# Optimization experiments

Measured on AMD Instinct MI355X. Metric: run time of the kernel, lower is better.

The kernel has to match this reference:

```python
import jax, jax.numpy as jnp
import numpy as np

N_NODES = 50000
N_EDGES = 1600000
N_GRAPHS = 512
IN_DIM = 384
HID = 128


def gcn_conv(x, W, b, src, dst, n_nodes):
    # PyG GCNConv: h = W^T x, then propagate with sym norm over A + I (self-loops).
    h = x @ W  # [N, out]
    # self-loops
    loop = jnp.arange(n_nodes, dtype=src.dtype)
    s = jnp.concatenate([src, loop])
    d = jnp.concatenate([dst, loop])
    ones = jnp.ones(s.shape[0], dtype=h.dtype)
    deg = jax.ops.segment_sum(ones, d, num_segments=n_nodes)  # in-degree incl self-loop
    dis = jnp.where(deg > 0, jax.lax.rsqrt(deg), 0.0)
    norm = dis[s] * dis[d]  # [E+N]
    msg = h[s] * norm[:, None]  # gather + scale
    out = jax.ops.segment_sum(msg, d, num_segments=n_nodes)  # scatter-add
    return out + b


def global_mean_pool(x, batch, num_graphs):
    sums = jax.ops.segment_sum(x, batch, num_segments=num_graphs)
    cnt = jax.ops.segment_sum(jnp.ones(x.shape[0], dtype=x.dtype), batch, num_segments=num_graphs)
    return sums / jnp.maximum(cnt, 1.0)[:, None]


def setup_inputs() -> dict:
    key = jax.random.key(0)
    ks = jax.random.split(key, 12)
    x = jax.random.normal(ks[0], (N_NODES, IN_DIM), dtype=jnp.float32)
    edge_index = jax.random.randint(ks[1], (2, N_EDGES), 0, N_NODES, dtype=jnp.int64 if jax.config.jax_enable_x64 else jnp.int32)
    batch = jnp.sort(jax.random.randint(ks[2], (N_NODES,), 0, N_GRAPHS, dtype=jnp.int32))
    def glorot(k, shape):
        lim = float(np.sqrt(6.0 / (shape[0] + shape[1])))
        return jax.random.uniform(k, shape, jnp.float32, -lim, lim)
    return {
        "x": x,
        "edge_index": edge_index,
        "batch": batch,
        "W1": glorot(ks[3], (IN_DIM, HID)),
        "b1": jnp.zeros((HID,), jnp.float32),
        "W2": glorot(ks[4], (HID, HID)),
        "b2": jnp.zeros((HID,), jnp.float32),
        "Wl1": glorot(ks[5], (HID, HID // 2)),
        "bl1": jnp.zeros((HID // 2,), jnp.float32),
        "Wl2": glorot(ks[6], (HID // 2, 5)),
        "bl2": jnp.zeros((5,), jnp.float32),
    }


def reference(x, edge_index, batch, W1, b1, W2, b2, Wl1, bl1, Wl2, bl2):
    src, dst = edge_index[0], edge_index[1]
    n = x.shape[0]
    h = jax.nn.relu(gcn_conv(x, W1, b1, src, dst, n))
    h = jax.nn.relu(gcn_conv(h, W2, b2, src, dst, n))
    g = global_mean_pool(h, batch, N_GRAPHS)  # [G, HID]
    g = jax.nn.relu(g @ Wl1 + bl1)
    return jax.nn.sigmoid(g @ Wl2 + bl2)  # [G, 5]
```

## Files before the change

kernel.cpp:

```cpp
#include <hip/hip_runtime.h>
#include <hip/hip_bf16.h>
#include <string.h>

#define HID 128
#define NGRAPH 512
#define IN_DIM 384

typedef __attribute__((ext_vector_type(2))) float f32x2;

__device__ __forceinline__ float bf2f(unsigned short u) {
    unsigned int x = ((unsigned int)u) << 16;
    float f; __builtin_memcpy(&f, &x, 4); return f;
}
__device__ __forceinline__ unsigned short f2bf(float f) {
    unsigned int b; __builtin_memcpy(&b, &f, 4);
    unsigned int r = (b + 0x7FFFu + ((b >> 16) & 1u)) >> 16;
    return (unsigned short)r;
}

__global__ void deg_kernel(const int* __restrict__ dst, int* __restrict__ deg, int E) {
    int e = blockIdx.x * blockDim.x + threadIdx.x;
    if (e < E) atomicAdd(&deg[dst[e]], 1);
}

__global__ void dis_kernel(const int* __restrict__ deg, float* __restrict__ dis, int n) {
    int v = blockIdx.x * blockDim.x + threadIdx.x;
    if (v < n) dis[v] = rsqrtf((float)(deg[v] + 1));
}

__global__ __launch_bounds__(256) void scan_part(const int* __restrict__ deg, int* __restrict__ row,
                                                 int* __restrict__ blockSums, int n) {
    __shared__ int ts[256];
    const int b = blockIdx.x, t = threadIdx.x;
    const int base = b * 1024 + t * 4;
    int v0 = (base + 0 < n) ? deg[base + 0] : 0;
    int v1 = (base + 1 < n) ? deg[base + 1] : 0;
    int v2 = (base + 2 < n) ? deg[base + 2] : 0;
    int v3 = (base + 3 < n) ? deg[base + 3] : 0;
    const int s = v0 + v1 + v2 + v3;
    ts[t] = s;
    __syncthreads();
    for (int off = 1; off < 256; off <<= 1) {
        int x = (t >= off) ? ts[t - off] : 0;
        __syncthreads();
        ts[t] += x;
        __syncthreads();
    }
    int p = ts[t] - s;
    if (base + 0 < n) { row[base + 0] = p; p += v0; }
    if (base + 1 < n) { row[base + 1] = p; p += v1; }
    if (base + 2 < n) { row[base + 2] = p; p += v2; }
    if (base + 3 < n) { row[base + 3] = p; }
    if (t == 255) blockSums[b] = ts[255];
}

__global__ void scan_tops(int* __restrict__ blockSums, int nb) {
    if (threadIdx.x == 0 && blockIdx.x == 0) {
        int acc = 0;
        for (int i = 0; i < nb; i++) { int v = blockSums[i]; blockSums[i] = acc; acc += v; }
    }
}

__global__ __launch_bounds__(256) void scan_add(int* __restrict__ row, int* __restrict__ cursor,
                                                const int* __restrict__ blockSums, int n, int E) {
    const int b = blockIdx.x, t = threadIdx.x;
    const int off = blockSums[b];
    const int base = b * 1024 + t * 4;
#pragma unroll
    for (int j = 0; j < 4; j++) {
        int i = base + j;
        if (i < n) { int v = row[i] + off; row[i] = v; cursor[i] = v; }
    }
    if (b == 0 && t == 0) row[n] = E;
}

__global__ void fill_kernel(const int* __restrict__ src, const int* __restrict__ dst,
                            int* __restrict__ cursor, unsigned short* __restrict__ csr16,
                            int E, int lo, int hi) {
    int e = blockIdx.x * blockDim.x + threadIdx.x;
    if (e < E) {
        const int d = dst[e];
        if (d >= lo && d < hi) {
            int pos = atomicAdd(&cursor[d], 1);
            csr16[pos] = (unsigned short)src[e];
        }
    }
}

template <int K, bool BF16IN>
__global__ __launch_bounds__(256) void gemm_tile(const void* __restrict__ Xv,
                                                 const float* __restrict__ W,
                                                 const float* __restrict__ dis,
                                                 unsigned int* __restrict__ out8, int n) {
    constexpr int KC = 32;
    __shared__ float asT[KC][68];
    __shared__ float bs[KC * HID];
    const int t = threadIdx.x;
    const int tx = t & 31;
    const int ty = t >> 5;
    const int row0 = blockIdx.x * 64;

    float4 acc[8];
#pragma unroll
    for (int j = 0; j < 8; j++) acc[j] = make_float4(0.f, 0.f, 0.f, 0.f);

    const int ar = t >> 3;
    const int af = t & 7;

    for (int k0 = 0; k0 < K; k0 += KC) {
#pragma unroll
        for (int half = 0; half < 2; half++) {
            const int r = ar + half * 32;
            const int gr = row0 + r;
            float4 a = make_float4(0.f, 0.f, 0.f, 0.f);
            if (gr < n) {
                if constexpr (BF16IN) {
                    const ushort4 u = *(const ushort4*)((const unsigned short*)Xv + (long)gr * K + k0 + af * 4);
                    a.x = bf2f(u.x); a.y = bf2f(u.y); a.z = bf2f(u.z); a.w = bf2f(u.w);
                } else {
                    a = *(const float4*)((const float*)Xv + (long)gr * K + k0 + af * 4);
                }
            }
            asT[af * 4 + 0][r] = a.x;
            asT[af * 4 + 1][r] = a.y;
            asT[af * 4 + 2][r] = a.z;
            asT[af * 4 + 3][r] = a.w;
        }
        {
            const float4* wp = (const float4*)&W[(long)k0 * HID];
            float4* bp = (float4*)bs;
#pragma unroll
            for (int i = 0; i < 4; i++) bp[t + i * 256] = wp[t + i * 256];
        }
        __syncthreads();
#pragma unroll 8
        for (int kk = 0; kk < KC; kk++) {
            const float4 a0 = *(const float4*)&asT[kk][ty * 8];
            const float4 a1 = *(const float4*)&asT[kk][ty * 8 + 4];
            const float4 b  = *(const float4*)&bs[kk * HID + tx * 4];
            acc[0].x = fmaf(a0.x, b.x, acc[0].x); acc[0].y = fmaf(a0.x, b.y, acc[0].y);
            acc[0].z = fmaf(a0.x, b.z, acc[0].z); acc[0].w = fmaf(a0.x, b.w, acc[0].w);
            acc[1].x = fmaf(a0.y, b.x, acc[1].x); acc[1].y = fmaf(a0.y, b.y, acc[1].y);
            acc[1].z = fmaf(a0.y, b.z, acc[1].z); acc[1].w = fmaf(a0.y, b.w, acc[1].w);
            acc[2].x = fmaf(a0.z, b.x, acc[2].x); acc[2].y = fmaf(a0.z, b.y, acc[2].y);
            acc[2].z = fmaf(a0.z, b.z, acc[2].z); acc[2].w = fmaf(a0.z, b.w, acc[2].w);
            acc[3].x = fmaf(a0.w, b.x, acc[3].x); acc[3].y = fmaf(a0.w, b.y, acc[3].y);
            acc[3].z = fmaf(a0.w, b.z, acc[3].z); acc[3].w = fmaf(a0.w, b.w, acc[3].w);
            acc[4].x = fmaf(a1.x, b.x, acc[4].x); acc[4].y = fmaf(a1.x, b.y, acc[4].y);
            acc[4].z = fmaf(a1.x, b.z, acc[4].z); acc[4].w = fmaf(a1.x, b.w, acc[4].w);
            acc[5].x = fmaf(a1.y, b.x, acc[5].x); acc[5].y = fmaf(a1.y, b.y, acc[5].y);
            acc[5].z = fmaf(a1.y, b.z, acc[5].z); acc[5].w = fmaf(a1.y, b.w, acc[5].w);
            acc[6].x = fmaf(a1.z, b.x, acc[6].x); acc[6].y = fmaf(a1.z, b.y, acc[6].y);
            acc[6].z = fmaf(a1.z, b.z, acc[6].z); acc[6].w = fmaf(a1.z, b.w, acc[6].w);
            acc[7].x = fmaf(a1.w, b.x, acc[7].x); acc[7].y = fmaf(a1.w, b.y, acc[7].y);
            acc[7].z = fmaf(a1.w, b.z, acc[7].z); acc[7].w = fmaf(a1.w, b.w, acc[7].w);
        }
        __syncthreads();
    }

#pragma unroll
    for (int j = 0; j < 8; j++) {
        const int v = row0 + ty * 8 + j;
        if (v < n) {
            const float s = dis[v] * 8.0f;
            int w01 = __builtin_amdgcn_cvt_pk_fp8_f32(acc[j].x * s, acc[j].y * s, 0, false);
            int w   = __builtin_amdgcn_cvt_pk_fp8_f32(acc[j].z * s, acc[j].w * s, w01, true);
            out8[(long)v * (HID / 4) + tx] = (unsigned int)w;
        }
    }
}

template <bool POOL>
__global__ __launch_bounds__(256) void agg_kernel(const unsigned char* __restrict__ hs8,
                                                  const unsigned short* __restrict__ csr16,
                                                  const int* __restrict__ row,
                                                  const float* __restrict__ dis,
                                                  const float* __restrict__ bias,
                                                  const int* __restrict__ batch,
                                                  unsigned int* __restrict__ buf,
                                                  float* __restrict__ sums,
                                                  int* __restrict__ cnt, int n) {
    const int v = blockIdx.x * 4 + (threadIdx.x >> 6);
    if (v >= n) return;
    const int lane = threadIdx.x & 63;
    const int sub = lane >> 3;
    const int lc  = lane & 7;

    const int rs = row[v];
    const int re = row[v + 1];

    float acc[16];
#pragma unroll
    for (int i = 0; i < 16; i++) acc[i] = 0.f;

    for (int base = rs; base < re; base += 32) {
        uint4 w[4];
        int vld[4];
#pragma unroll
        for (int p = 0; p < 4; p++) {
            const int pe = base + p * 8;
            if (pe < re) {
                const int ei = pe + sub;
                const int idx = __builtin_nontemporal_load(&csr16[(ei < re) ? ei : (re - 1)]);
                w[p] = *(const uint4*)&hs8[(long)idx * HID + (lc << 4)];
                vld[p] = (ei < re);
            } else {
                w[p] = make_uint4(0u, 0u, 0u, 0u);
                vld[p] = 0;
            }
        }
#pragma unroll
        for (int p = 0; p < 4; p++) {
            if (vld[p]) {
                const uint4 ww = w[p];
                f32x2 u;
                u = __builtin_amdgcn_cvt_pk_f32_fp8(ww.x, false); acc[0]  += u.x; acc[1]  += u.y;
                u = __builtin_amdgcn_cvt_pk_f32_fp8(ww.x, true);  acc[2]  += u.x; acc[3]  += u.y;
                u = __builtin_amdgcn_cvt_pk_f32_fp8(ww.y, false); acc[4]  += u.x; acc[5]  += u.y;
                u = __builtin_amdgcn_cvt_pk_f32_fp8(ww.y, true);  acc[6]  += u.x; acc[7]  += u.y;
                u = __builtin_amdgcn_cvt_pk_f32_fp8(ww.z, false); acc[8]  += u.x; acc[9]  += u.y;
                u = __builtin_amdgcn_cvt_pk_f32_fp8(ww.z, true);  acc[10] += u.x; acc[11] += u.y;
                u = __builtin_amdgcn_cvt_pk_f32_fp8(ww.w, false); acc[12] += u.x; acc[13] += u.y;
                u = __builtin_amdgcn_cvt_pk_f32_fp8(ww.w, true);  acc[14] += u.x; acc[15] += u.y;
            }
        }
    }

#pragma unroll
    for (int i = 0; i < 16; i++) {
        acc[i] += __shfl_xor(acc[i], 8, 64);
        acc[i] += __shfl_xor(acc[i], 16, 64);
        acc[i] += __shfl_xor(acc[i], 32, 64);
    }

    const int col = (lc << 4) + (sub << 1);
    const unsigned short selfw = *(const unsigned short*)&hs8[(long)v * HID + col];
    f32x2 sf = __builtin_amdgcn_cvt_pk_f32_fp8((unsigned int)selfw, false);
    const float sx = acc[(sub << 1) + 0] + sf.x;
    const float sy = acc[(sub << 1) + 1] + sf.y;
    const float dv = dis[v] * 0.125f;
    const float rx = fmaxf(fmaf(dv, sx, bias[col]), 0.f);
    const float ry = fmaxf(fmaf(dv, sy, bias[col + 1]), 0.f);
    if (POOL) {
        const int g = batch[v];
        unsafeAtomicAdd(&sums[g * HID + col], rx);
        unsafeAtomicAdd(&sums[g * HID + col + 1], ry);
        if (lane == 0) atomicAdd(&cnt[g], 1);
    } else {
        const unsigned int pk = (unsigned int)f2bf(rx) | ((unsigned int)f2bf(ry) << 16);
        buf[(long)v * (HID / 2) + (col >> 1)] = pk;
    }
}

__global__ __launch_bounds__(64) void mlp_kernel(const float* __restrict__ sums,
                                                 const int* __restrict__ cnt,
                                                 const float* __restrict__ Wl1,
                                                 const float* __restrict__ bl1,
                                                 const float* __restrict__ Wl2,
                                                 const float* __restrict__ bl2,
                                                 float* __restrict__ out) {
    const int g = blockIdx.x, t = threadIdx.x;
    __shared__ float mean[HID];
    __shared__ float hid[64];
    const float c = fmaxf((float)cnt[g], 1.0f);
    mean[t] = sums[g * HID + t] / c;
    mean[t + 64] = sums[g * HID + 64 + t] / c;
    __syncthreads();
    float acc = bl1[t];
#pragma unroll 4
    for (int k = 0; k < HID; k++) acc = fmaf(mean[k], Wl1[k * 64 + t], acc);
    hid[t] = fmaxf(acc, 0.f);
    __syncthreads();
    if (t < 5) {
        float a = bl2[t];
#pragma unroll 4
        for (int k = 0; k < 64; k++) a = fmaf(hid[k], Wl2[k * 5 + t], a);
        out[g * 5 + t] = 1.f / (1.f + expf(-a));
    }
}

extern "C" void kernel_launch(void* const* d_in, const int* in_sizes, int n_in,
                              void* d_out, int out_size, void* d_ws, size_t ws_size,
                              hipStream_t stream) {
    const float* x   = (const float*)d_in[0];
    const int* ei    = (const int*)d_in[1];
    const int* batch = (const int*)d_in[2];
    const float* W1  = (const float*)d_in[3];
    const float* b1  = (const float*)d_in[4];
    const float* W2  = (const float*)d_in[5];
    const float* b2  = (const float*)d_in[6];
    const float* Wl1 = (const float*)d_in[7];
    const float* bl1 = (const float*)d_in[8];
    const float* Wl2 = (const float*)d_in[9];
    const float* bl2 = (const float*)d_in[10];
    float* out = (float*)d_out;

    const int n = in_sizes[0] / IN_DIM;
    const int E = in_sizes[1] / 2;
    const int* src = ei;
    const int* dst = ei + E;

    char* ws = (char*)d_ws;
    size_t off = 0;
    auto alloc = [&](size_t bytes) {
        void* p = ws + off;
        off = (off + bytes + 255) & ~(size_t)255;
        return p;
    };
    int*   deg       = (int*)alloc((size_t)n * 4);
    float* dis       = (float*)alloc((size_t)n * 4);
    int*   row       = (int*)alloc((size_t)(n + 1) * 4);
    int*   cursor    = (int*)alloc((size_t)n * 4);
    unsigned short* csr16 = (unsigned short*)alloc((size_t)E * 2);
    int*   blockSums = (int*)alloc(256 * 4);
    unsigned char* hs8 = (unsigned char*)alloc((size_t)n * HID);
    unsigned int* buf1 = (unsigned int*)alloc((size_t)n * HID * 2);
    float* sums = (float*)alloc((size_t)NGRAPH * HID * 4);
    int*   cnt  = (int*)alloc((size_t)NGRAPH * 4);
    (void)ws_size;

    const int nb = (n + 1023) / 1024;
    const int gemmBlocks = (n + 63) / 64;
    const int aggBlocks  = (n + 3) / 4;
    const int edgeBlocks = (E + 255) / 256;

    hipMemsetAsync(deg, 0, (size_t)n * 4, stream);
    hipMemsetAsync(sums, 0, (size_t)NGRAPH * HID * 4 + (size_t)NGRAPH * 4, stream);

    deg_kernel<<<edgeBlocks, 256, 0, stream>>>(dst, deg, E);
    dis_kernel<<<(n + 255) / 256, 256, 0, stream>>>(deg, dis, n);
    scan_part<<<nb, 256, 0, stream>>>(deg, row, blockSums, n);
    scan_tops<<<1, 64, 0, stream>>>(blockSums, nb);
    scan_add<<<nb, 256, 0, stream>>>(row, cursor, blockSums, n, E);
    {
        const int step = (n + 3) / 4;
        for (int k = 0; k < 4; k++) {
            const int lo = k * step;
            const int hi = (k == 3) ? n : (lo + step);
            fill_kernel<<<edgeBlocks, 256, 0, stream>>>(src, dst, cursor, csr16, E, lo, hi);
        }
    }

    gemm_tile<IN_DIM, false><<<gemmBlocks, 256, 0, stream>>>(x, W1, dis, (unsigned int*)hs8, n);
    agg_kernel<false><<<aggBlocks, 256, 0, stream>>>(hs8, csr16, row, dis, b1, batch,
                                                     buf1, nullptr, nullptr, n);

    gemm_tile<HID, true><<<gemmBlocks, 256, 0, stream>>>(buf1, W2, dis, (unsigned int*)hs8, n);
    agg_kernel<true><<<aggBlocks, 256, 0, stream>>>(hs8, csr16, row, dis, b2, batch,
                                                    nullptr, sums, cnt, n);

    mlp_kernel<<<NGRAPH, 64, 0, stream>>>(sums, cnt, Wl1, bl1, Wl2, bl2, out);
}
```

Measured before the change: 584.7 us.

## Replace FP32 SIMT GEMM with bf16 MFMA GEMM and prepacked weights

Replaces the scalar-FMA tiled GEMM with a bf16 MFMA 16x16x32 kernel. Weights are converted once per call into an MFMA-friendly packed bf16 layout by a new pack_w kernel. Input activations are converted to bf16 on load and staged through swizzled shared memory. The epilogue goes through shared memory so the existing fp8 output layout is kept. The dis computation is also folded into scan_part, which removes one launch. The trade-off is lower GEMM input precision (bf16 instead of fp32) plus an extra small launch for packing.

```diff
diff --git a/kernel.cpp b/kernel.cpp
--- a/kernel.cpp
+++ b/kernel.cpp
@@ -7,11 +7,9 @@
 #define IN_DIM 384
 
 typedef __attribute__((ext_vector_type(2))) float f32x2;
-
-__device__ __forceinline__ float bf2f(unsigned short u) {
-    unsigned int x = ((unsigned int)u) << 16;
-    float f; __builtin_memcpy(&f, &x, 4); return f;
-}
+typedef __attribute__((ext_vector_type(4))) float f32x4;
+typedef __attribute__((ext_vector_type(8))) short short8v;
+
 __device__ __forceinline__ unsigned short f2bf(float f) {
     unsigned int b; __builtin_memcpy(&b, &f, 4);
     unsigned int r = (b + 0x7FFFu + ((b >> 16) & 1u)) >> 16;
@@ -23,13 +21,36 @@
     if (e < E) atomicAdd(&deg[dst[e]], 1);
 }
 
-__global__ void dis_kernel(const int* __restrict__ deg, float* __restrict__ dis, int n) {
-    int v = blockIdx.x * blockDim.x + threadIdx.x;
-    if (v < n) dis[v] = rsqrtf((float)(deg[v] + 1));
+__global__ __launch_bounds__(256) void pack_w(const float* __restrict__ W1,
+                                              const float* __restrict__ W2,
+                                              unsigned short* __restrict__ w8_1,
+                                              unsigned short* __restrict__ w8_2) {
+    const int f = blockIdx.x * 256 + threadIdx.x;
+    const int F1 = (IN_DIM / 32) * 8 * 64;
+    const int F2 = (HID / 32) * 8 * 64;
+    if (f >= F1 + F2) return;
+    const float* W = (f < F1) ? W1 : W2;
+    unsigned short* o = (f < F1) ? w8_1 : w8_2;
+    const int fl = (f < F1) ? f : (f - F1);
+    const int kc = fl >> 9;
+    const int nt = (fl >> 6) & 7;
+    const int l  = fl & 63;
+    const int kb = kc * 32 + ((l >> 4) << 3);
+    const int col = nt * 16 + (l & 15);
+    unsigned int u0 = (unsigned int)f2bf(W[(long)(kb + 0) * HID + col]) |
+                      ((unsigned int)f2bf(W[(long)(kb + 1) * HID + col]) << 16);
+    unsigned int u1 = (unsigned int)f2bf(W[(long)(kb + 2) * HID + col]) |
+                      ((unsigned int)f2bf(W[(long)(kb + 3) * HID + col]) << 16);
+    unsigned int u2 = (unsigned int)f2bf(W[(long)(kb + 4) * HID + col]) |
+                      ((unsigned int)f2bf(W[(long)(kb + 5) * HID + col]) << 16);
+    unsigned int u3 = (unsigned int)f2bf(W[(long)(kb + 6) * HID + col]) |
+                      ((unsigned int)f2bf(W[(long)(kb + 7) * HID + col]) << 16);
+    *(uint4*)&o[(size_t)fl * 8] = make_uint4(u0, u1, u2, u3);
 }
 
 __global__ __launch_bounds__(256) void scan_part(const int* __restrict__ deg, int* __restrict__ row,
-                                                 int* __restrict__ blockSums, int n) {
+                                                 int* __restrict__ blockSums, float* __restrict__ dis,
+                                                 int n) {
     __shared__ int ts[256];
     const int b = blockIdx.x, t = threadIdx.x;
     const int base = b * 1024 + t * 4;
@@ -37,6 +58,10 @@
     int v1 = (base + 1 < n) ? deg[base + 1] : 0;
     int v2 = (base + 2 < n) ? deg[base + 2] : 0;
     int v3 = (base + 3 < n) ? deg[base + 3] : 0;
+    if (base + 0 < n) dis[base + 0] = rsqrtf((float)(v0 + 1));
+    if (base + 1 < n) dis[base + 1] = rsqrtf((float)(v1 + 1));
+    if (base + 2 < n) dis[base + 2] = rsqrtf((float)(v2 + 1));
+    if (base + 3 < n) dis[base + 3] = rsqrtf((float)(v3 + 1));
     const int s = v0 + v1 + v2 + v3;
     ts[t] = s;
     __syncthreads();
@@ -88,84 +113,88 @@
 }
 
 template <int K, bool BF16IN>
-__global__ __launch_bounds__(256) void gemm_tile(const void* __restrict__ Xv,
-                                                 const float* __restrict__ W,
+__global__ __launch_bounds__(256) void gemm_mfma(const void* __restrict__ Xv,
+                                                 const unsigned short* __restrict__ w8,
                                                  const float* __restrict__ dis,
                                                  unsigned int* __restrict__ out8, int n) {
-    constexpr int KC = 32;
-    __shared__ float asT[KC][68];
-    __shared__ float bs[KC * HID];
+    __shared__ __align__(16) unsigned char smem[64 * 132 * 4];
+    float* eps = (float*)smem;
+
     const int t = threadIdx.x;
-    const int tx = t & 31;
-    const int ty = t >> 5;
+    const int lane = t & 63;
+    const int wave = t >> 6;
     const int row0 = blockIdx.x * 64;
 
-    float4 acc[8];
-#pragma unroll
-    for (int j = 0; j < 8; j++) acc[j] = make_float4(0.f, 0.f, 0.f, 0.f);
-
-    const int ar = t >> 3;
-    const int af = t & 7;
-
-    for (int k0 = 0; k0 < K; k0 += KC) {
-#pragma unroll
-        for (int half = 0; half < 2; half++) {
-            const int r = ar + half * 32;
-            const int gr = row0 + r;
-            float4 a = make_float4(0.f, 0.f, 0.f, 0.f);
+    f32x4 acc[8];
+#pragma unroll
+    for (int i = 0; i < 8; i++) acc[i] = (f32x4){0.f, 0.f, 0.f, 0.f};
+
+    const int sr = t >> 2;
+    const int sq = t & 3;
+    const int sw_byte = ((sr * 64 + sq * 16) ^ ((sr & 7) << 4));
+    const int am = (wave << 4) + (lane & 15);
+    const int ac = lane >> 4;
+    const int ard_byte = ((am * 64 + ac * 16) ^ ((am & 7) << 4));
+
+    const int nsteps = K / 32;
+    for (int ks = 0; ks < nsteps; ++ks) {
+        const int k0 = ks * 32;
+        {
+            const int gr = row0 + sr;
+            unsigned int u0 = 0, u1 = 0, u2 = 0, u3 = 0;
             if (gr < n) {
                 if constexpr (BF16IN) {
-                    const ushort4 u = *(const ushort4*)((const unsigned short*)Xv + (long)gr * K + k0 + af * 4);
-                    a.x = bf2f(u.x); a.y = bf2f(u.y); a.z = bf2f(u.z); a.w = bf2f(u.w);
+                    const uint4 b = *(const uint4*)((const unsigned short*)Xv + (size_t)gr * K + k0 + sq * 8);
+                    u0 = b.x; u1 = b.y; u2 = b.z; u3 = b.w;
                 } else {
-                    a = *(const float4*)((const float*)Xv + (long)gr * K + k0 + af * 4);
+                    const float4 x0 = *(const float4*)((const float*)Xv + (size_t)gr * K + k0 + sq * 8);
+                    const float4 x1 = *(const float4*)((const float*)Xv + (size_t)gr * K + k0 + sq * 8 + 4);
+                    u0 = (unsigned int)f2bf(x0.x) | ((unsigned int)f2bf(x0.y) << 16);
+                    u1 = (unsigned int)f2bf(x0.z) | ((unsigned int)f2bf(x0.w) << 16);
+                    u2 = (unsigned int)f2bf(x1.x) | ((unsigned int)f2bf(x1.y) << 16);
+                    u3 = (unsigned int)f2bf(x1.z) | ((unsigned int)f2bf(x1.w) << 16);
                 }
             }
-            asT[af * 4 + 0][r] = a.x;
-            asT[af * 4 + 1][r] = a.y;
-            asT[af * 4 + 2][r] = a.z;
-            asT[af * 4 + 3][r] = a.w;
-        }
+            *(uint4*)(smem + sw_byte) = make_uint4(u0, u1, u2, u3);
+        }
+        __syncthreads();
         {
-            const float4* wp = (const float4*)&W[(long)k0 * HID];
-            float4* bp = (float4*)bs;
-#pragma unroll
-            for (int i = 0; i < 4; i++) bp[t + i * 256] = wp[t + i * 256];
+            const short8v a = *(const short8v*)(smem + ard_byte);
+            const unsigned short* wp = w8 + ((size_t)(ks * 8) * 64 + lane) * 8;
+#pragma unroll
+            for (int nt = 0; nt < 8; ++nt) {
+                const short8v b = *(const short8v*)(wp + (size_t)nt * 64 * 8);
+                acc[nt] = __builtin_amdgcn_mfma_f32_16x16x32_bf16(a, b, acc[nt], 0, 0, 0);
+            }
         }
         __syncthreads();
-#pragma unroll 8
-        for (int kk = 0; kk < KC; kk++) {
-            const float4 a0 = *(const float4*)&asT[kk][ty * 8];
-            const float4 a1 = *(const float4*)&asT[kk][ty * 8 + 4];
-            const float4 b  = *(const float4*)&bs[kk * HID + tx * 4];
-            acc[0].x = fmaf(a0.x, b.x, acc[0].x); acc[0].y = fmaf(a0.x, b.y, acc[0].y);
-            acc[0].z = fmaf(a0.x, b.z, acc[0].z); acc[0].w = fmaf(a0.x, b.w, acc[0].w);
-            acc[1].x = fmaf(a0.y, b.x, acc[1].x); acc[1].y = fmaf(a0.y, b.y, acc[1].y);
-            acc[1].z = fmaf(a0.y, b.z, acc[1].z); acc[1].w = fmaf(a0.y, b.w, acc[1].w);
-            acc[2].x = fmaf(a0.z, b.x, acc[2].x); acc[2].y = fmaf(a0.z, b.y, acc[2].y);
-            acc[2].z = fmaf(a0.z, b.z, acc[2].z); acc[2].w = fmaf(a0.z, b.w, acc[2].w);
-            acc[3].x = fmaf(a0.w, b.x, acc[3].x); acc[3].y = fmaf(a0.w, b.y, acc[3].y);
-            acc[3].z = fmaf(a0.w, b.z, acc[3].z); acc[3].w = fmaf(a0.w, b.w, acc[3].w);
-            acc[4].x = fmaf(a1.x, b.x, acc[4].x); acc[4].y = fmaf(a1.x, b.y, acc[4].y);
-            acc[4].z = fmaf(a1.x, b.z, acc[4].z); acc[4].w = fmaf(a1.x, b.w, acc[4].w);
-            acc[5].x = fmaf(a1.y, b.x, acc[5].x); acc[5].y = fmaf(a1.y, b.y, acc[5].y);
-            acc[5].z = fmaf(a1.y, b.z, acc[5].z); acc[5].w = fmaf(a1.y, b.w, acc[5].w);
-            acc[6].x = fmaf(a1.z, b.x, acc[6].x); acc[6].y = fmaf(a1.z, b.y, acc[6].y);
-            acc[6].z = fmaf(a1.z, b.z, acc[6].z); acc[6].w = fmaf(a1.z, b.w, acc[6].w);
-            acc[7].x = fmaf(a1.w, b.x, acc[7].x); acc[7].y = fmaf(a1.w, b.y, acc[7].y);
-            acc[7].z = fmaf(a1.w, b.z, acc[7].z); acc[7].w = fmaf(a1.w, b.w, acc[7].w);
-        }
-        __syncthreads();
-    }
-
-#pragma unroll
-    for (int j = 0; j < 8; j++) {
-        const int v = row0 + ty * 8 + j;
-        if (v < n) {
-            const float s = dis[v] * 8.0f;
-            int w01 = __builtin_amdgcn_cvt_pk_fp8_f32(acc[j].x * s, acc[j].y * s, 0, false);
-            int w   = __builtin_amdgcn_cvt_pk_fp8_f32(acc[j].z * s, acc[j].w * s, w01, true);
-            out8[(long)v * (HID / 4) + tx] = (unsigned int)w;
+    }
+
+    {
+        const int er = (wave << 4) + ((lane >> 4) << 2);
+        const int ec = lane & 15;
+#pragma unroll
+        for (int nt = 0; nt < 8; ++nt) {
+#pragma unroll
+            for (int r = 0; r < 4; ++r) {
+                eps[(size_t)(er + r) * 132 + nt * 16 + ec] = acc[nt][r];
+            }
+        }
+    }
+    __syncthreads();
+    {
+        const int tx = t & 31;
+        const int ty = t >> 5;
+#pragma unroll
+        for (int j = 0; j < 8; ++j) {
+            const int v = row0 + ty * 8 + j;
+            if (v < n) {
+                const float4 a4 = *(const float4*)&eps[(size_t)(ty * 8 + j) * 132 + tx * 4];
+                const float s = dis[v] * 8.0f;
+                int w01 = __builtin_amdgcn_cvt_pk_fp8_f32(a4.x * s, a4.y * s, 0, false);
+                int w   = __builtin_amdgcn_cvt_pk_fp8_f32(a4.z * s, a4.w * s, w01, true);
+                out8[(size_t)v * (HID / 4) + tx] = (unsigned int)w;
+            }
         }
     }
 }
@@ -315,6 +344,8 @@
     int*   blockSums = (int*)alloc(256 * 4);
     unsigned char* hs8 = (unsigned char*)alloc((size_t)n * HID);
     unsigned int* buf1 = (unsigned int*)alloc((size_t)n * HID * 2);
+    unsigned short* w8_1 = (unsigned short*)alloc((size_t)IN_DIM * HID * 2);
+    unsigned short* w8_2 = (unsigned short*)alloc((size_t)HID * HID * 2);
     float* sums = (float*)alloc((size_t)NGRAPH * HID * 4);
     int*   cnt  = (int*)alloc((size_t)NGRAPH * 4);
     (void)ws_size;
@@ -327,9 +358,10 @@
     hipMemsetAsync(deg, 0, (size_t)n * 4, stream);
     hipMemsetAsync(sums, 0, (size_t)NGRAPH * HID * 4 + (size_t)NGRAPH * 4, stream);
 
+    pack_w<<<32, 256, 0, stream>>>(W1, W2, w8_1, w8_2);
+
     deg_kernel<<<edgeBlocks, 256, 0, stream>>>(dst, deg, E);
-    dis_kernel<<<(n + 255) / 256, 256, 0, stream>>>(deg, dis, n);
-    scan_part<<<nb, 256, 0, stream>>>(deg, row, blockSums, n);
+    scan_part<<<nb, 256, 0, stream>>>(deg, row, blockSums, dis, n);
     scan_tops<<<1, 64, 0, stream>>>(blockSums, nb);
     scan_add<<<nb, 256, 0, stream>>>(row, cursor, blockSums, n, E);
     {
@@ -341,11 +373,11 @@
         }
     }
 
-    gemm_tile<IN_DIM, false><<<gemmBlocks, 256, 0, stream>>>(x, W1, dis, (unsigned int*)hs8, n);
+    gemm_mfma<IN_DIM, false><<<gemmBlocks, 256, 0, stream>>>(x, w8_1, dis, (unsigned int*)hs8, n);
     agg_kernel<false><<<aggBlocks, 256, 0, stream>>>(hs8, csr16, row, dis, b1, batch,
                                                      buf1, nullptr, nullptr, n);
 
-    gemm_tile<HID, true><<<gemmBlocks, 256, 0, stream>>>(buf1, W2, dis, (unsigned int*)hs8, n);
+    gemm_mfma<HID, true><<<gemmBlocks, 256, 0, stream>>>(buf1, w8_2, dis, (unsigned int*)hs8, n);
     agg_kernel<true><<<aggBlocks, 256, 0, stream>>>(hs8, csr16, row, dis, b2, batch,
                                                     nullptr, sums, cnt, n);
 
```

After: 528.6 us. 9.6% less time.
